# Optimization experiments

Hardware: AMD Instinct MI355X
Metric: run time of the kernel (lower is better)

The kernel has to match this reference:

```python
import jax, jax.numpy as jnp
import numpy as np

B, S, E, H = 2, 2048, 1024, 16
Dh = E // H  # 64
KEEP = 0.9   # 1 - dropout_p
INV_SCALE = 1.0  # forward() default; call site does not pass inv_scale


def setup_inputs() -> dict:
    key = jax.random.key(0)
    ks = jax.random.split(key, 12)
    query = jax.random.normal(ks[0], (B, S, E), dtype=jnp.float32)
    key_t = jax.random.normal(ks[1], (B, S, E), dtype=jnp.float32)
    value = jax.random.normal(ks[2], (B, S, E), dtype=jnp.float32)
    attn_mask = jax.random.randint(ks[3], (B, S), 0, 2, dtype=jnp.int32)
    # pre-scaled inverted dropout keep-mask (deterministic stand-in for F.dropout)
    dropout_mask = (jax.random.uniform(ks[4], (B, H, S, S)) < KEEP).astype(jnp.float32) / KEEP
    Wq = jax.random.normal(ks[5], (E, E), dtype=jnp.float32) * 0.02
    bq = jnp.zeros((E,), dtype=jnp.float32)
    Wk = jax.random.normal(ks[6], (E, E), dtype=jnp.float32) * 0.02
    bk = jnp.zeros((E,), dtype=jnp.float32)
    Wv = jax.random.normal(ks[7], (E, E), dtype=jnp.float32) * 0.02
    bv = jnp.zeros((E,), dtype=jnp.float32)
    return {"query": query, "key": key_t, "value": value, "attn_mask": attn_mask,
            "dropout_mask": dropout_mask, "Wq": Wq, "bq": bq, "Wk": Wk, "bk": bk,
            "Wv": Wv, "bv": bv}


def _heads(x, W, b):
    # Linear then split heads: (B,S,E) -> (B,H,S,Dh)
    y = x @ W.T + b
    return y.reshape(B, S, H, Dh).transpose(0, 2, 1, 3)


def reference(query, key, value, attn_mask, dropout_mask, Wq, bq, Wk, bk, Wv, bv):
    q = _heads(query, Wq, bq)
    k = _heads(key, Wk, bk)
    v = _heads(value, Wv, bv)
    scores = jnp.einsum("bhqd,bhkd->bhqk", q, k) / INV_SCALE
    pad = (attn_mask == 0)[:, None, None, :]  # (B,1,1,S) True = masked
    scores = jnp.where(pad, -jnp.inf, scores)
    attn = jax.nn.softmax(scores, axis=-1) * dropout_mask
    out = jnp.einsum("bhqk,bhkd->bhqd", attn, v)  # (B,H,S,Dh)
    return out
```

## Files before the change

### kernel.cpp

```cpp
#include <hip/hip_runtime.h>

#define B_ 2
#define S_ 2048
#define E_ 1024
#define H_ 16
#define DH 64
#define MM (B_*S_)
#define BHN (B_*H_)

typedef unsigned short u16;
typedef unsigned int u32;
typedef __attribute__((ext_vector_type(8))) __bf16 bf16x8;
typedef __attribute__((ext_vector_type(8))) _Float16 f16x8;
typedef __attribute__((ext_vector_type(4))) float f32x4;
typedef __attribute__((ext_vector_type(8))) u16 u16x8;
typedef __attribute__((ext_vector_type(4))) u16 u16x4;

static __device__ __forceinline__ u16 f2bf(float f) {
  u32 u = __builtin_bit_cast(u32, f);
  u += 0x7fffu + ((u >> 16) & 1u);
  return (u16)(u >> 16);
}
static __device__ __forceinline__ float bf2f(u16 h) {
  return __builtin_bit_cast(float, (u32)h << 16);
}
static __device__ __forceinline__ u32 sw(u32 byte) {
  return byte ^ (((byte >> 7) & 7u) << 4);
}
static __device__ __forceinline__ bf16x8 frag(const u16* lds, u32 byte) {
  return *(const bf16x8*)((const char*)lds + byte);
}
static __device__ __forceinline__ f16x8 frag16(const u16* lds, u32 byte) {
  return *(const f16x8*)((const char*)lds + byte);
}
static __device__ __forceinline__ f32x4 mfma_bf(bf16x8 a, bf16x8 b, f32x4 c) {
  return __builtin_amdgcn_mfma_f32_16x16x32_bf16(a, b, c, 0, 0, 0);
}
static __device__ __forceinline__ f32x4 mfma_f16(f16x8 a, f16x8 b, f32x4 c) {
  return __builtin_amdgcn_mfma_f32_16x16x32_f16(a, b, c, 0, 0, 0);
}
static __device__ __forceinline__ void gload_lds16(const u16* g, u16* lds_base) {
  __builtin_amdgcn_global_load_lds(
      (const __attribute__((address_space(1))) u32*)g,
      (__attribute__((address_space(3))) u32*)lds_base, 16, 0, 0);
}

#define L2E 1.44269504088896340736f

struct SplitArg { const float* s; u16* h; u16* l; int n4; };

__global__ void split6_kernel(SplitArg a0, SplitArg a1, SplitArg a2,
                              SplitArg a3, SplitArg a4, SplitArg a5) {
  SplitArg A = (blockIdx.z == 0) ? a0 : (blockIdx.z == 1) ? a1 : (blockIdx.z == 2) ? a2
             : (blockIdx.z == 3) ? a3 : (blockIdx.z == 4) ? a4 : a5;
  int i = blockIdx.x * blockDim.x + threadIdx.x;
  int stride = gridDim.x * blockDim.x;
  if (A.l) {
    for (; i < A.n4; i += stride) {
      float4 v = ((const float4*)A.s)[i];
      u16x4 h, l;
      h.x = f2bf(v.x); l.x = f2bf(v.x - bf2f(h.x));
      h.y = f2bf(v.y); l.y = f2bf(v.y - bf2f(h.y));
      h.z = f2bf(v.z); l.z = f2bf(v.z - bf2f(h.z));
      h.w = f2bf(v.w); l.w = f2bf(v.w - bf2f(h.w));
      ((u16x4*)A.h)[i] = h;
      ((u16x4*)A.l)[i] = l;
    }
  } else {
    for (; i < A.n4; i += stride) {
      float4 v = ((const float4*)A.s)[i];
      u16x4 h;
      h.x = f2bf(v.x); h.y = f2bf(v.y); h.z = f2bf(v.z); h.w = f2bf(v.w);
      ((u16x4*)A.h)[i] = h;
    }
  }
}

__global__ void pack_mask(const int* __restrict__ am, u32* __restrict__ pm) {
  int w = threadIdx.x;
  if (w < 128) {
    int base = (w >> 6) * 2048 + (w & 63) * 32;
    u32 bits = 0;
#pragma unroll
    for (int j = 0; j < 8; ++j) {
      int4 v = *(const int4*)(am + base + j * 4);
      bits |= (v.x ? 1u : 0u) << (4 * j) | (v.y ? 1u : 0u) << (4 * j + 1) |
              (v.z ? 1u : 0u) << (4 * j + 2) | (v.w ? 1u : 0u) << (4 * j + 3);
    }
    pm[w] = bits;
  }
}

struct ProjArgs {
  const u16* xhi; const u16* xlo; const u16* whi; const u16* wlo;
  const float* bias; u16* ohi; int mode;
};

__global__ __launch_bounds__(256, 3) void proj_gemm(ProjArgs a0, ProjArgs a1, ProjArgs a2) {
  ProjArgs A = (blockIdx.z == 0) ? a0 : (blockIdx.z == 1) ? a1 : a2;
  __shared__ u16 As[128 * 64];
  __shared__ u16 Bs[128 * 64];
  const int t = threadIdx.x;
  const int l = t & 63, wid = t >> 6;
  const int g = l >> 4, ln = l & 15;
  const int wm = wid >> 1, wn = wid & 1;
  int bid = blockIdx.y * 8 + blockIdx.x;
  int sid = (bid & 7) * 32 + (bid >> 3);
  const int m0 = (sid >> 3) * 128, e0 = (sid & 7) * 128;

  f32x4 acc[4][4] = {};
  const int nkt = (A.mode == 2) ? 32 : 48;

  for (int kt = 0; kt < nkt; ++kt) {
    int kp = kt * 64;
    const u16* asrc = (kp < 2048) ? A.xhi : A.xlo;
    const u16* bsrc = (kp < 1024 || kp >= 2048) ? A.whi : A.wlo;
    int kc = kp & 1023;
#pragma unroll
    for (int r = 0; r < 4; ++r) {
      int cr = wid * 4 + r;
      int row = cr * 8 + (l >> 3);
      int col = (l & 7) * 8;
      gload_lds16(asrc + (size_t)(m0 + row) * 1024 + kc + col, As + cr * 512);
      gload_lds16(bsrc + (size_t)(e0 + row) * 1024 + kc + col, Bs + cr * 512);
    }
    __syncthreads();
#pragma unroll
    for (int ks = 0; ks < 2; ++ks) {
      bf16x8 af[4], bfv[4];
#pragma unroll
      for (int i = 0; i < 4; ++i) {
        af[i] = frag(As, (u32)(wm * 64 + i * 16 + ln) * 128 + ks * 64 + g * 16);
        bfv[i] = frag(Bs, (u32)(wn * 64 + i * 16 + ln) * 128 + ks * 64 + g * 16);
      }
#pragma unroll
      for (int i = 0; i < 4; ++i)
#pragma unroll
        for (int j = 0; j < 4; ++j)
          acc[i][j] = mfma_bf(af[i], bfv[j], acc[i][j]);
    }
    __syncthreads();
  }

#pragma unroll
  for (int i = 0; i < 4; ++i) {
#pragma unroll
    for (int j = 0; j < 4; ++j) {
      int e = e0 + wn * 64 + j * 16 + ln;
      int h = e >> 6, d = e & 63;
      float bias = A.bias[e];
      if (A.mode < 2) {
#pragma unroll
        for (int r = 0; r < 4; ++r) {
          int m = m0 + wm * 64 + i * 16 + g * 4 + r;
          float v = acc[i][j][r] + bias;
          if (A.mode == 0) v *= L2E;
          int b = m >> 11, s = m & 2047;
          size_t idx = ((size_t)((b * 16 + h) * 2048 + s)) * 64 + d;
          A.ohi[idx] = __builtin_bit_cast(u16, (_Float16)v);
        }
      } else {
        int m = m0 + wm * 64 + i * 16 + g * 4;
        int b = m >> 11, s = m & 2047;
        u16x4 pv;
#pragma unroll
        for (int r = 0; r < 4; ++r)
          pv[r] = __builtin_bit_cast(u16, (__bf16)(acc[i][j][r] + bias));
        size_t idx = ((size_t)((b * 16 + h) * 64 + d)) * 2048 + s;
        *(u16x4*)(A.ohi + idx) = pv;
      }
    }
  }
}

__global__ __launch_bounds__(256, 3) void attn_kernel(
    const u16* __restrict__ qf, const u16* __restrict__ kf,
    const u16* __restrict__ vt, const u32* __restrict__ pm,
    const float* __restrict__ dmask, float* __restrict__ out) {
  __shared__ u16 Ks[2][64 * 64];
  __shared__ u16 Vs[2][64 * 64];
  __shared__ u16 Ps[4 * 16 * 64];

  const int t = threadIdx.x, l = t & 63, wid = t >> 6;
  const int g = l >> 4, ln = l & 15;

  int bid = blockIdx.y * 32 + blockIdx.x;
  int sid = (bid & 7) * 128 + (bid >> 3);
  const int qt = sid & 31, bh = sid >> 5, b = bh >> 4;
  const int q0 = qt * 64;
  const int qrow = q0 + wid * 16 + ln;
  const size_t qg = ((size_t)bh * 2048 + qrow) * 64;
  const u32* pmb = pm + b * 64;

  f16x8 qv[2];
#pragma unroll
  for (int ks = 0; ks < 2; ++ks)
    qv[ks] = *(const f16x8*)(qf + qg + ks * 32 + g * 8);

  const float* dmp = dmask + ((size_t)bh * 2048 + qrow) * 2048 + 4 * g;
  const int c0 = wid * 64 + l, c1 = wid * 64 + 256 + l;
  const int s0 = c0 ^ ((c0 >> 3) & 7), s1 = c1 ^ ((c1 >> 3) & 7);
  const u16* kp0 = kf + (size_t)bh * 2048 * 64 + s0 * 8;
  const u16* kp1 = kf + (size_t)bh * 2048 * 64 + s1 * 8;
  const u16* vp0 = vt + ((size_t)bh * 64 + (s0 >> 3)) * 2048 + (s0 & 7) * 8;
  const u16* vp1 = vt + ((size_t)bh * 64 + (s1 >> 3)) * 2048 + (s1 & 7) * 8;

  auto stage = [&](int buf, int kt) {
    gload_lds16(kp0 + (size_t)kt * 4096, Ks[buf] + c0 * 8 - l * 8 + l * 8);
  };
  (void)stage;

  auto stage_tile = [&](int buf, int kt) {
    u16* kd = Ks[buf];
    u16* vd = Vs[buf];
    gload_lds16(kp0 + (size_t)kt * 4096, kd + (wid * 64) * 8);
    gload_lds16(kp1 + (size_t)kt * 4096, kd + (wid * 64 + 256) * 8);
    gload_lds16(vp0 + kt * 64, vd + (wid * 64) * 8);
    gload_lds16(vp1 + kt * 64, vd + (wid * 64 + 256) * 8);
  };

  float4 dmc[4], dmn[4];
#pragma unroll
  for (int i = 0; i < 4; ++i) dmc[i] = *(const float4*)(dmp + i * 16);

  stage_tile(0, 0);
  __syncthreads();

  f32x4 O[4] = {};
  float Zacc = 0.f;
  const u32 psbase = (u32)(wid * 2048 + ln * 128);
  u32 pw[4], pr[2];
#pragma unroll
  for (int i = 0; i < 4; ++i) pw[i] = sw(psbase + i * 32 + g * 8);
#pragma unroll
  for (int ks = 0; ks < 2; ++ks) pr[ks] = sw(psbase + ks * 64 + g * 16);

  for (int kt = 0; kt < 32; ++kt) {
    const int buf = kt & 1;
    if (kt < 31) {
      stage_tile(buf ^ 1, kt + 1);
      const float* dmn_p = dmp + (kt + 1) * 64;
#pragma unroll
      for (int i = 0; i < 4; ++i) dmn[i] = *(const float4*)(dmn_p + i * 16);
    }
    u32 m0 = pmb[2 * kt], m1 = pmb[2 * kt + 1];

    f32x4 sc[4] = {};
#pragma unroll
    for (int ks = 0; ks < 2; ++ks) {
#pragma unroll
      for (int i = 0; i < 4; ++i) {
        f16x8 ak = frag16(Ks[buf], sw((u32)((i * 16 + ln) * 128 + ks * 64 + g * 16)));
        sc[i] = mfma_f16(ak, qv[ks], sc[i]);
      }
    }

#pragma unroll
    for (int i = 0; i < 4; ++i) {
      u32 mm = (i < 2 ? m0 : m1) >> (((i & 1) << 4) + 4 * g);
      float e0 = (mm & 1u) ? exp2f(sc[i][0]) : 0.f;
      float e1 = (mm & 2u) ? exp2f(sc[i][1]) : 0.f;
      float e2 = (mm & 4u) ? exp2f(sc[i][2]) : 0.f;
      float e3 = (mm & 8u) ? exp2f(sc[i][3]) : 0.f;
      Zacc += (e0 + e1) + (e2 + e3);
      u16x4 p;
      p.x = __builtin_bit_cast(u16, (__bf16)(e0 * dmc[i].x));
      p.y = __builtin_bit_cast(u16, (__bf16)(e1 * dmc[i].y));
      p.z = __builtin_bit_cast(u16, (__bf16)(e2 * dmc[i].z));
      p.w = __builtin_bit_cast(u16, (__bf16)(e3 * dmc[i].w));
      *(u16x4*)((char*)Ps + pw[i]) = p;
    }

#pragma unroll
    for (int ks = 0; ks < 2; ++ks) {
      bf16x8 bP = frag(Ps, pr[ks]);
#pragma unroll
      for (int id = 0; id < 4; ++id) {
        bf16x8 aV = frag(Vs[buf], sw((u32)((id * 16 + ln) * 128 + ks * 64 + g * 16)));
        O[id] = mfma_bf(aV, bP, O[id]);
      }
    }

    __syncthreads();
    if (kt < 31) {
#pragma unroll
      for (int i = 0; i < 4; ++i) dmc[i] = dmn[i];
    }
  }

  float z = Zacc;
  z += __shfl_xor(z, 16, 64);
  z += __shfl_xor(z, 32, 64);
  float rz = 1.f / z;

#pragma unroll
  for (int id = 0; id < 4; ++id) {
    float4 o;
    o.x = O[id][0] * rz; o.y = O[id][1] * rz;
    o.z = O[id][2] * rz; o.w = O[id][3] * rz;
    *(float4*)(out + qg + id * 16 + 4 * g) = o;
  }
}

extern "C" void kernel_launch(void* const* d_in, const int* in_sizes, int n_in,
                              void* d_out, int out_size, void* d_ws, size_t ws_size,
                              hipStream_t stream) {
  const float* query = (const float*)d_in[0];
  const float* keyt  = (const float*)d_in[1];
  const float* value = (const float*)d_in[2];
  const int*   amask = (const int*)d_in[3];
  const float* dmask = (const float*)d_in[4];
  const float* Wq = (const float*)d_in[5];
  const float* bq = (const float*)d_in[6];
  const float* Wk = (const float*)d_in[7];
  const float* bk = (const float*)d_in[8];
  const float* Wv = (const float*)d_in[9];
  const float* bv = (const float*)d_in[10];

  char* ws = (char*)d_ws;
  size_t off = 0;
  auto alloc = [&](size_t bytes) {
    char* p = ws + off;
    off += (bytes + 255) & ~(size_t)255;
    return p;
  };
  const size_t XB = (size_t)MM * E_ * sizeof(u16);
  const size_t WB = (size_t)E_ * E_ * sizeof(u16);

  u16 *xh[3], *xl[3], *wh[3], *wl[3];
  for (int i = 0; i < 3; ++i) { xh[i] = (u16*)alloc(XB); xl[i] = (u16*)alloc(XB); }
  for (int i = 0; i < 3; ++i) { wh[i] = (u16*)alloc(WB); wl[i] = (u16*)alloc(WB); }
  u16* q_f16 = (u16*)alloc(XB);
  u16* k_f16 = (u16*)alloc(XB);
  u16* v_t   = (u16*)alloc(XB);
  u32* pmask = (u32*)alloc(512);
  if (off > ws_size) return;

  SplitArg sa[6] = {
      {query, xh[0], xl[0], MM * E_ / 4}, {keyt, xh[1], xl[1], MM * E_ / 4},
      {value, xh[2], nullptr, MM * E_ / 4}, {Wq, wh[0], wl[0], E_ * E_ / 4},
      {Wk, wh[1], wl[1], E_ * E_ / 4},    {Wv, wh[2], wl[2], E_ * E_ / 4},
  };
  split6_kernel<<<dim3(512, 1, 6), 256, 0, stream>>>(sa[0], sa[1], sa[2], sa[3], sa[4], sa[5]);
  pack_mask<<<1, 128, 0, stream>>>(amask, pmask);

  ProjArgs pa[3] = {
      {xh[0], xl[0], wh[0], wl[0], bq, q_f16, 0},
      {xh[1], xl[1], wh[1], wl[1], bk, k_f16, 1},
      {xh[2], nullptr, wh[2], wl[2], bv, v_t, 2},
  };
  proj_gemm<<<dim3(8, 32, 3), 256, 0, stream>>>(pa[0], pa[1], pa[2]);

  attn_kernel<<<dim3(32, 32), 256, 0, stream>>>(
      q_f16, k_f16, v_t, pmask, dmask, (float*)d_out);
}
```

Before: 294.1 us.

## Split attention over key dimension into four chunks with a combine kernel

Splits the key loop of the attention kernel into four chunks along a third grid dimension. Each block writes an unnormalized partial output and a partial softmax denominator to workspace, and a new combine kernel sums the partials and normalizes. This raises the block count from 1024 to 4096 to improve occupancy and load balance across CUs. The cost is extra workspace traffic for the partials, one more kernel launch, and repeated Q loads and prologue per chunk.

```diff
diff --git a/kernel.cpp b/kernel.cpp
--- a/kernel.cpp
+++ b/kernel.cpp
@@ -7,6 +7,7 @@
 #define DH 64
 #define MM (B_*S_)
 #define BHN (B_*H_)
+#define KSPLIT 4
 
 typedef unsigned short u16;
 typedef unsigned int u32;
@@ -176,7 +177,8 @@
 __global__ __launch_bounds__(256, 3) void attn_kernel(
     const u16* __restrict__ qf, const u16* __restrict__ kf,
     const u16* __restrict__ vt, const u32* __restrict__ pm,
-    const float* __restrict__ dmask, float* __restrict__ out) {
+    const float* __restrict__ dmask, float* __restrict__ opart,
+    float* __restrict__ zpart) {
   __shared__ u16 Ks[2][64 * 64];
   __shared__ u16 Vs[2][64 * 64];
   __shared__ u16 Ps[4 * 16 * 64];
@@ -187,6 +189,7 @@
   int bid = blockIdx.y * 32 + blockIdx.x;
   int sid = (bid & 7) * 128 + (bid >> 3);
   const int qt = sid & 31, bh = sid >> 5, b = bh >> 4;
+  const int kc = blockIdx.z;
   const int q0 = qt * 64;
   const int qrow = q0 + wid * 16 + ln;
   const size_t qg = ((size_t)bh * 2048 + qrow) * 64;
@@ -205,25 +208,21 @@
   const u16* vp0 = vt + ((size_t)bh * 64 + (s0 >> 3)) * 2048 + (s0 & 7) * 8;
   const u16* vp1 = vt + ((size_t)bh * 64 + (s1 >> 3)) * 2048 + (s1 & 7) * 8;
 
-  auto stage = [&](int buf, int kt) {
-    gload_lds16(kp0 + (size_t)kt * 4096, Ks[buf] + c0 * 8 - l * 8 + l * 8);
-  };
-  (void)stage;
-
-  auto stage_tile = [&](int buf, int kt) {
+  auto stage_tile = [&](int buf, int kt2) {
     u16* kd = Ks[buf];
     u16* vd = Vs[buf];
-    gload_lds16(kp0 + (size_t)kt * 4096, kd + (wid * 64) * 8);
-    gload_lds16(kp1 + (size_t)kt * 4096, kd + (wid * 64 + 256) * 8);
-    gload_lds16(vp0 + kt * 64, vd + (wid * 64) * 8);
-    gload_lds16(vp1 + kt * 64, vd + (wid * 64 + 256) * 8);
+    gload_lds16(kp0 + (size_t)kt2 * 4096, kd + (wid * 64) * 8);
+    gload_lds16(kp1 + (size_t)kt2 * 4096, kd + (wid * 64 + 256) * 8);
+    gload_lds16(vp0 + kt2 * 64, vd + (wid * 64) * 8);
+    gload_lds16(vp1 + kt2 * 64, vd + (wid * 64 + 256) * 8);
   };
 
   float4 dmc[4], dmn[4];
-#pragma unroll
-  for (int i = 0; i < 4; ++i) dmc[i] = *(const float4*)(dmp + i * 16);
-
-  stage_tile(0, 0);
+  const float* dm0 = dmp + kc * 8 * 64;
+#pragma unroll
+  for (int i = 0; i < 4; ++i) dmc[i] = *(const float4*)(dm0 + i * 16);
+
+  stage_tile(0, kc * 8);
   __syncthreads();
 
   f32x4 O[4] = {};
@@ -235,15 +234,16 @@
 #pragma unroll
   for (int ks = 0; ks < 2; ++ks) pr[ks] = sw(psbase + ks * 64 + g * 16);
 
-  for (int kt = 0; kt < 32; ++kt) {
+  for (int kt = 0; kt < 8; ++kt) {
     const int buf = kt & 1;
-    if (kt < 31) {
-      stage_tile(buf ^ 1, kt + 1);
-      const float* dmn_p = dmp + (kt + 1) * 64;
+    const int kt2 = kc * 8 + kt;
+    if (kt < 7) {
+      stage_tile(buf ^ 1, kt2 + 1);
+      const float* dmn_p = dmp + (kt2 + 1) * 64;
 #pragma unroll
       for (int i = 0; i < 4; ++i) dmn[i] = *(const float4*)(dmn_p + i * 16);
     }
-    u32 m0 = pmb[2 * kt], m1 = pmb[2 * kt + 1];
+    u32 m0 = pmb[2 * kt2], m1 = pmb[2 * kt2 + 1];
 
     f32x4 sc[4] = {};
 #pragma unroll
@@ -282,7 +282,7 @@
     }
 
     __syncthreads();
-    if (kt < 31) {
+    if (kt < 7) {
 #pragma unroll
       for (int i = 0; i < 4; ++i) dmc[i] = dmn[i];
     }
@@ -291,15 +291,35 @@
   float z = Zacc;
   z += __shfl_xor(z, 16, 64);
   z += __shfl_xor(z, 32, 64);
-  float rz = 1.f / z;
-
+  const int row = bh * 2048 + qrow;
+  if (g == 0) zpart[kc * (BHN * S_) + row] = z;
+
+  float* opb = opart + ((size_t)kc * (BHN * S_) + row) * 64;
 #pragma unroll
   for (int id = 0; id < 4; ++id) {
     float4 o;
-    o.x = O[id][0] * rz; o.y = O[id][1] * rz;
-    o.z = O[id][2] * rz; o.w = O[id][3] * rz;
-    *(float4*)(out + qg + id * 16 + 4 * g) = o;
-  }
+    o.x = O[id][0]; o.y = O[id][1]; o.z = O[id][2]; o.w = O[id][3];
+    *(float4*)(opb + id * 16 + 4 * g) = o;
+  }
+}
+
+__global__ void combine_kernel(const float* __restrict__ op,
+                               const float* __restrict__ zp,
+                               float* __restrict__ out) {
+  int tid = blockIdx.x * blockDim.x + threadIdx.x;
+  int row = tid >> 4, d4 = tid & 15;
+  float4 o = make_float4(0.f, 0.f, 0.f, 0.f);
+  float z = 0.f;
+#pragma unroll
+  for (int kc = 0; kc < KSPLIT; ++kc) {
+    float4 v = *(const float4*)(op + ((size_t)kc * (BHN * S_) + row) * 64 + d4 * 4);
+    o.x += v.x; o.y += v.y; o.z += v.z; o.w += v.w;
+    z += zp[kc * (BHN * S_) + row];
+  }
+  float rz = 1.f / z;
+  float4 r;
+  r.x = o.x * rz; r.y = o.y * rz; r.z = o.z * rz; r.w = o.w * rz;
+  *(float4*)(out + (size_t)row * 64 + d4 * 4) = r;
 }
 
 extern "C" void kernel_launch(void* const* d_in, const int* in_sizes, int n_in,
@@ -334,6 +354,8 @@
   u16* k_f16 = (u16*)alloc(XB);
   u16* v_t   = (u16*)alloc(XB);
   u32* pmask = (u32*)alloc(512);
+  float* opart = (float*)alloc((size_t)KSPLIT * BHN * S_ * 64 * 4);
+  float* zpart = (float*)alloc((size_t)KSPLIT * BHN * S_ * 4);
   if (off > ws_size) return;
 
   SplitArg sa[6] = {
@@ -351,6 +373,9 @@
   };
   proj_gemm<<<dim3(8, 32, 3), 256, 0, stream>>>(pa[0], pa[1], pa[2]);
 
-  attn_kernel<<<dim3(32, 32), 256, 0, stream>>>(
-      q_f16, k_f16, v_t, pmask, dmask, (float*)d_out);
-}
+  attn_kernel<<<dim3(32, 32, KSPLIT), 256, 0, stream>>>(
+      q_f16, k_f16, v_t, pmask, dmask, opart, zpart);
+
+  combine_kernel<<<(BHN * S_ * 64 / 4) / 256, 256, 0, stream>>>(
+      opart, zpart, (float*)d_out);
+}
```

Measured after the change: 284.5 us. 3.3% less time.
